# Kernel optimization log

Measured on AMD Instinct MI355X. Metric: run time of the kernel, lower is better.

The kernel has to match this reference:

```python
import jax, jax.numpy as jnp
import numpy as np

N, E, H, R = 20000, 320000, 64, 32
CUTOFF = 5.0
EYE3 = jnp.eye(3, dtype=jnp.float32)


def _decompose(X):
    # X: [..., 3, 3] -> (I trace part, A antisymmetric, S traceless symmetric)
    tr = jnp.trace(X, axis1=-2, axis2=-1)
    I = tr[..., None, None] / 3.0 * EYE3
    A = (X - jnp.swapaxes(X, -1, -2)) / 2.0
    S = (X + jnp.swapaxes(X, -1, -2)) / 2.0 - I
    return I, A, S


def _tnorm(X):
    return (X ** 2).sum((-2, -1))


def _mix(T, W):
    # channel-wise Linear without bias: Linear applied after permute(0,2,3,1)
    return jnp.einsum('nhij,gh->ngij', T, W)


def setup_inputs() -> dict:
    key = jax.random.key(0)
    ks = jax.random.split(key, 8)
    s = 0.05
    X = jax.random.normal(ks[0], (N, H, 3, 3), jnp.float32)
    edge_index = jax.random.randint(ks[1], (2, E), 0, N, dtype=jnp.int64)
    edge_dist = jax.random.uniform(ks[2], (E,), jnp.float32) * CUTOFF
    edge_attr = jax.random.normal(ks[3], (E, R), jnp.float32)
    w1 = jax.random.normal(ks[4], (H, R), jnp.float32) * s
    b1 = jnp.zeros((H,), jnp.float32)
    w2 = jax.random.normal(ks[5], (2 * H, H), jnp.float32) * s
    b2 = jnp.zeros((2 * H,), jnp.float32)
    w3 = jax.random.normal(ks[6], (3 * H, 2 * H), jnp.float32) * s
    b3 = jnp.zeros((3 * H,), jnp.float32)
    lin_w = jax.random.normal(ks[7], (6, H, H), jnp.float32) * s
    return dict(X=X, edge_index=edge_index, edge_dist=edge_dist, edge_attr=edge_attr,
                w1=w1, b1=b1, w2=w2, b2=b2, w3=w3, b3=b3, lin_w=lin_w)


def reference(X, edge_index, edge_dist, edge_attr, w1, b1, w2, b2, w3, b3, lin_w):
    row, col = edge_index[0], edge_index[1]
    # CosineCutoff: 0.5*(cos(pi*d/cutoff)+1) inside cutoff
    C = 0.5 * (jnp.cos(edge_dist * (jnp.pi / CUTOFF)) + 1.0) * (edge_dist < CUTOFF).astype(edge_dist.dtype)
    h = jax.nn.silu(edge_attr @ w1.T + b1)
    h = jax.nn.silu(h @ w2.T + b2)
    edge_feat = ((h @ w3.T + b3) * C[:, None]).reshape(E, H, 3)
    Xn = X / (_tnorm(X) + 1.0)[..., None, None]
    I, A, S = _decompose(Xn)
    I = _mix(I, lin_w[0])
    A = _mix(A, lin_w[1])
    S = _mix(S, lin_w[2])
    Y = I + A + S

    def msg(f, T):  # gather tensor[col], weight by edge factor, scatter-add to row
        return jax.ops.segment_sum(f[:, :, None, None] * T[col], row, num_segments=N)

    M = msg(edge_feat[..., 0], I) + msg(edge_feat[..., 1], A) + msg(edge_feat[..., 2], S)
    prod = jnp.matmul(M, Y) + jnp.matmul(Y, M)  # O(3) branch
    I2, A2, S2 = _decompose(prod)
    norm = (_tnorm(I2 + A2 + S2) + 1.0)[..., None, None]
    dX = _mix(I2 / norm, lin_w[3]) + _mix(A2 / norm, lin_w[4]) + _mix(S2 / norm, lin_w[5])
    return Xn + dX + jnp.matmul(dX, dX)
```

## Files before the change

### kernel.cpp

```cpp
#include <hip/hip_runtime.h>
#include <hip/hip_fp16.h>
#include <hip/hip_bf16.h>

#define NR 32

typedef __attribute__((ext_vector_type(8))) short bf8_t;
typedef __attribute__((ext_vector_type(4))) float f4_t;

__device__ __forceinline__ float silu_f(float x) {
    return x * __builtin_amdgcn_rcpf(1.0f + __expf(-x));
}

__device__ __forceinline__ unsigned pkbf(float lo, float hi) {
    __hip_bfloat162 h = __float22bfloat162_rn(make_float2(lo, hi));
    union { __hip_bfloat162 h2; unsigned u; } cv; cv.h2 = h; return cv.u;
}
__device__ __forceinline__ float bf_lo(unsigned u) { return __uint_as_float(u << 16); }
__device__ __forceinline__ float bf_hi(unsigned u) { return __uint_as_float(u & 0xffff0000u); }

__device__ __forceinline__ float rdl(float v, int l) {
    return __int_as_float(__builtin_amdgcn_readlane(__float_as_int(v), l));
}

__global__ __launch_bounds__(256) void k_hist(
    const int* __restrict__ eidx, int* __restrict__ cnt, int nedges)
{
    int e = blockIdx.x * 256 + threadIdx.x;
    if (e < nedges) atomicAdd(&cnt[eidx[e]], 1);
}

__global__ __launch_bounds__(256) void k_scatter(
    const int* __restrict__ eidx, int* __restrict__ cur,
    int* __restrict__ perm, int* __restrict__ col_s, int nedges)
{
    int e = blockIdx.x * 256 + threadIdx.x;
    if (e < nedges) {
        int r = eidx[e];
        int pos = atomicAdd(&cur[r], 1);
        perm[pos] = e;
        col_s[pos] = eidx[nedges + e];
    }
}

__global__ __launch_bounds__(512) void k_mega(
    int* __restrict__ cnt, int* __restrict__ off, int nnodes,
    const float* __restrict__ w1, const float* __restrict__ b1,
    const float* __restrict__ w2, const float* __restrict__ b2,
    const float* __restrict__ w3, const float* __restrict__ b3,
    unsigned* __restrict__ wpre,
    const float* __restrict__ X, const float* __restrict__ lw,
    unsigned* __restrict__ Tmh, int nk1blocks)
{
    __shared__ float Wl[3 * 64 * 68];
    const int tid = threadIdx.x;
    const int bid = blockIdx.x;

    if (bid == 0) {
        int* ish = (int*)Wl;
        const int lane = tid & 63, wid = tid >> 6;
        const int n = nnodes;
        const int per = (n + 511) >> 9;
        const int base = tid * per;
        int s = 0;
        for (int i = 0; i < per; i++) {
            int idx = base + i;
            if (idx < n) s += cnt[idx];
        }
        int incl = s;
        for (int d = 1; d < 64; d <<= 1) {
            int t = __shfl_up(incl, d);
            if (lane >= d) incl += t;
        }
        if (lane == 63) ish[wid] = incl;
        __syncthreads();
        if (wid == 0) {
            int v = (lane < 8) ? ish[lane] : 0;
            int inc2 = v;
            for (int d = 1; d < 8; d <<= 1) {
                int t = __shfl_up(inc2, d);
                if (lane >= d) inc2 += t;
            }
            if (lane < 8) ish[8 + lane] = inc2 - v;
            if (lane == 7) off[n] = inc2;
        }
        __syncthreads();
        int run = ish[8 + wid] + incl - s;
        for (int i = 0; i < per; i++) {
            int idx = base + i;
            if (idx < n) {
                int v = cnt[idx];
                off[idx] = run;
                cnt[idx] = run;
                run += v;
            }
        }
        return;
    }

    if (bid > nk1blocks) {
        int i = (bid - nk1blocks - 1) * 512 + tid;
        if (i < 12288) {
            int mk = i >> 8, m = mk >> 2, kt = mk & 3;
            int rr = (i >> 4) & 15, gg = (i >> 2) & 3, dd = i & 3;
            int row = 16 * m + rr;
            int c0 = 32 * kt + 16 * (dd >> 1) + 4 * gg + 2 * (dd & 1);
            const float* s = w3 + (size_t)row * 128 + c0;
            wpre[i] = pkbf(s[0], s[1]);
        } else if (i < 12672) {
            int j = i - 12288;
            float v = (j < 64) ? b1[j] : (j < 192) ? b2[j - 64] : b3[j - 192];
            wpre[i] = __float_as_uint(v);
        } else if (i < 13696) {
            int j = i - 12672;
            int m = j >> 8, rr = (j >> 4) & 15, gg = (j >> 2) & 3, dd = j & 3;
            const float* s = w1 + (size_t)(16 * m + rr) * 32 + 8 * gg + 2 * dd;
            wpre[i] = pkbf(s[0], s[1]);
        } else if (i < 17792) {
            int j = i - 13696;
            int mk = j >> 8, m = mk >> 1, kt = mk & 1;
            int rr = (j >> 4) & 15, gg = (j >> 2) & 3, dd = j & 3;
            int row = 16 * m + rr;
            int c0 = 32 * kt + 16 * (dd >> 1) + 4 * gg + 2 * (dd & 1);
            const float* s = w2 + (size_t)row * 64 + c0;
            wpre[i] = pkbf(s[0], s[1]);
        }
        return;
    }

#pragma unroll
    for (int k = 0; k < 6; k++) {
        int l = (tid + k * 512) * 4;
        int row = l >> 6, col = l & 63;
        *(float4*)&Wl[row * 68 + col] = *(const float4*)(lw + l);
    }

    const int wid = tid >> 6, lane = tid & 63;
    const int n = (bid - 1) * 8 + wid;
    const bool valid = (n < nnodes);

    float i0 = 0, i1 = 0, i2 = 0, i3 = 0, i4 = 0, i5 = 0, i6 = 0, i7 = 0, i8 = 0;
    if (valid) {
        const float* xp = X + ((size_t)n * 64 + lane) * 9;
        float v[9];
#pragma unroll
        for (int i = 0; i < 9; i++) v[i] = xp[i];
        float tn = 0.f;
#pragma unroll
        for (int i = 0; i < 9; i++) tn = fmaf(v[i], v[i], tn);
        float inv = 1.0f / (tn + 1.0f);
#pragma unroll
        for (int i = 0; i < 9; i++) v[i] *= inv;
        float lam = (v[0] + v[4] + v[8]) * (1.0f / 3.0f);
        i0 = lam;
        i1 = (v[1] - v[3]) * 0.5f;
        i2 = (v[2] - v[6]) * 0.5f;
        i3 = (v[5] - v[7]) * 0.5f;
        i4 = v[0] - lam;
        i5 = (v[1] + v[3]) * 0.5f;
        i6 = (v[2] + v[6]) * 0.5f;
        i7 = v[4] - lam;
        i8 = (v[5] + v[7]) * 0.5f;
    }
    __syncthreads();

    const int g = lane;
    float a0 = 0, a1 = 0, a2 = 0, a3 = 0, a4 = 0, a5 = 0, a6 = 0, a7 = 0, a8 = 0;
#pragma unroll
    for (int h4 = 0; h4 < 64; h4 += 4) {
        float4 w0 = *(const float4*)&Wl[g * 68 + h4];
        float4 w1v = *(const float4*)&Wl[(64 + g) * 68 + h4];
        float4 w2v = *(const float4*)&Wl[(128 + g) * 68 + h4];
#pragma unroll
        for (int j = 0; j < 4; j++) {
            const int h = h4 + j;
            float wa = (&w0.x)[j], wb = (&w1v.x)[j], wc = (&w2v.x)[j];
            a0 = fmaf(wa, rdl(i0, h), a0);
            a1 = fmaf(wb, rdl(i1, h), a1);
            a2 = fmaf(wb, rdl(i2, h), a2);
            a3 = fmaf(wb, rdl(i3, h), a3);
            a4 = fmaf(wc, rdl(i4, h), a4);
            a5 = fmaf(wc, rdl(i5, h), a5);
            a6 = fmaf(wc, rdl(i6, h), a6);
            a7 = fmaf(wc, rdl(i7, h), a7);
            a8 = fmaf(wc, rdl(i8, h), a8);
        }
    }
    if (valid) {
        unsigned* outp = Tmh + (size_t)n * 320 + g;
        outp[0 * 64] = pkbf(a0, a1);
        outp[1 * 64] = pkbf(a2, a3);
        outp[2 * 64] = pkbf(a4, a5);
        outp[3 * 64] = pkbf(a6, a7);
        outp[4 * 64] = pkbf(a8, 0.f);
    }
}

#define LBI 49152
#define LW1P 50688
#define LW2P 54784
#define LEF 71168
#define EFS 408
#define NW  14

__global__
__attribute__((amdgpu_flat_work_group_size(896, 896)))
__attribute__((amdgpu_waves_per_eu(3)))
void k2f_fused(
    const float* __restrict__ ea, const float* __restrict__ dist,
    const int* __restrict__ perm, const int* __restrict__ col_s,
    const int* __restrict__ off, const unsigned* __restrict__ wpre,
    const unsigned* __restrict__ Tmh, float* __restrict__ out, int nrows)
{
    __shared__ __align__(16) char smem[LEF + NW * 16 * EFS];
    const int tid = threadIdx.x;

#pragma unroll
    for (int k = 0; k < 5; k++) {
        int idx = tid + k * 896;
        if (idx < 4448)
            ((uint4*)smem)[idx] = ((const uint4*)wpre)[idx];
    }

    const int wid = tid >> 6, lane = tid & 63;
    const int r16 = lane & 15, g = lane >> 4;
    const int slot = r16 * 4 + g;
    char* efb = smem + LEF + wid * (16 * EFS);
    __syncthreads();

    const int r = blockIdx.x * NW + wid;
    if (r >= nrows) return;
    const int beg = off[r];
    const int deg = off[r + 1] - beg;

    float acc[9];
#pragma unroll
    for (int i = 0; i < 9; i++) acc[i] = 0.f;

#pragma unroll 1
    for (int c0 = 0; c0 < deg; c0 += 16) {
        const int cnt = min(16, deg - c0);

        int colv = col_s[beg + c0 + ((r16 < cnt) ? r16 : (cnt - 1))];
        int e = perm[beg + c0 + ((r16 < cnt) ? r16 : 0)];
        const float* ar = ea + (size_t)e * NR + 8 * g;
        float4 v0 = *(const float4*)(ar);
        float4 v1 = *(const float4*)(ar + 4);
        float d = dist[e];

        bf8_t bx;
        {
            union { bf8_t v; unsigned u[4]; } tt;
            tt.u[0] = pkbf(v0.x, v0.y); tt.u[1] = pkbf(v0.z, v0.w);
            tt.u[2] = pkbf(v1.x, v1.y); tt.u[3] = pkbf(v1.z, v1.w);
            bx = tt.v;
        }
        float cf = (r16 < cnt && d < 5.0f)
                 ? 0.5f * (__cosf(d * 0.62831853071795864f) + 1.0f) : 0.0f;

        unsigned pk1[4][2];
#pragma unroll
        for (int m = 0; m < 4; m++) {
            f4_t c = *(const f4_t*)(smem + LBI + (16 * m + 4 * g) * 4);
            bf8_t aw = *(const bf8_t*)(smem + LW1P + (m * 64 + slot) * 16);
            c = __builtin_amdgcn_mfma_f32_16x16x32_bf16(aw, bx, c, 0, 0, 0);
            pk1[m][0] = pkbf(silu_f(c[0]), silu_f(c[1]));
            pk1[m][1] = pkbf(silu_f(c[2]), silu_f(c[3]));
        }
        bf8_t B2[2];
        {
            union { bf8_t v; unsigned u[4]; } ta, tb;
            ta.u[0] = pk1[0][0]; ta.u[1] = pk1[0][1]; ta.u[2] = pk1[1][0]; ta.u[3] = pk1[1][1];
            tb.u[0] = pk1[2][0]; tb.u[1] = pk1[2][1]; tb.u[2] = pk1[3][0]; tb.u[3] = pk1[3][1];
            B2[0] = ta.v; B2[1] = tb.v;
        }

        unsigned pk2[8][2];
#pragma unroll
        for (int m = 0; m < 8; m++) {
            f4_t c = *(const f4_t*)(smem + LBI + (64 + 16 * m + 4 * g) * 4);
#pragma unroll
            for (int kt = 0; kt < 2; kt++) {
                bf8_t aw = *(const bf8_t*)(smem + LW2P + ((m * 2 + kt) * 64 + slot) * 16);
                c = __builtin_amdgcn_mfma_f32_16x16x32_bf16(aw, B2[kt], c, 0, 0, 0);
            }
            pk2[m][0] = pkbf(silu_f(c[0]), silu_f(c[1]));
            pk2[m][1] = pkbf(silu_f(c[2]), silu_f(c[3]));
        }
        bf8_t B3[4];
#pragma unroll
        for (int kt = 0; kt < 4; kt++) {
            union { bf8_t v; unsigned u[4]; } tt;
            tt.u[0] = pk2[2 * kt][0]; tt.u[1] = pk2[2 * kt][1];
            tt.u[2] = pk2[2 * kt + 1][0]; tt.u[3] = pk2[2 * kt + 1][1];
            B3[kt] = tt.v;
        }

        asm volatile("s_waitcnt lgkmcnt(0)" ::: "memory");
        __builtin_amdgcn_sched_barrier(0);

#pragma unroll
        for (int m = 0; m < 12; m++) {
            f4_t c = *(const f4_t*)(smem + LBI + (192 + 16 * m + 4 * g) * 4);
#pragma unroll
            for (int kt = 0; kt < 4; kt++) {
                bf8_t aw = *(const bf8_t*)(smem + ((m * 4 + kt) * 64 + slot) * 16);
                c = __builtin_amdgcn_mfma_f32_16x16x32_bf16(aw, B3[kt], c, 0, 0, 0);
            }
            union { struct { __half2 a, b; } h; uint2 u; } pu;
            pu.h.a = __float22half2_rn(make_float2(c[0] * cf, c[1] * cf));
            pu.h.b = __float22half2_rn(make_float2(c[2] * cf, c[3] * cf));
            *(uint2*)(efb + r16 * EFS + (16 * m + 4 * g) * 2) = pu.u;
        }
        asm volatile("s_waitcnt lgkmcnt(0)" ::: "memory");
        __builtin_amdgcn_sched_barrier(0);

        unsigned q[4][5];
#pragma unroll
        for (int s = 0; s < 4; s++) {
            int sc = __builtin_amdgcn_readlane(colv, s);
            const unsigned* t = Tmh + (size_t)(unsigned)sc * 320 + lane;
            q[s][0] = t[0]; q[s][1] = t[64]; q[s][2] = t[128];
            q[s][3] = t[192]; q[s][4] = t[256];
        }

#define ACC_STEP(S, Q)                                                        \
        {                                                                     \
            const __half* fp = (const __half*)(efb + (S) * EFS + 6 * lane);   \
            float f0 = __half2float(fp[0]);                                   \
            float f1 = __half2float(fp[1]);                                   \
            float f2 = __half2float(fp[2]);                                   \
            acc[0] = fmaf(f0, bf_lo(Q[0]), acc[0]);                           \
            acc[1] = fmaf(f1, bf_hi(Q[0]), acc[1]);                           \
            acc[2] = fmaf(f1, bf_lo(Q[1]), acc[2]);                           \
            acc[3] = fmaf(f1, bf_hi(Q[1]), acc[3]);                           \
            acc[4] = fmaf(f2, bf_lo(Q[2]), acc[4]);                           \
            acc[5] = fmaf(f2, bf_hi(Q[2]), acc[5]);                           \
            acc[6] = fmaf(f2, bf_lo(Q[3]), acc[6]);                           \
            acc[7] = fmaf(f2, bf_hi(Q[3]), acc[7]);                           \
            acc[8] = fmaf(f2, bf_lo(Q[4]), acc[8]);                           \
        }
#define LOAD_Q(DST, S)                                                        \
        {                                                                     \
            int sc = __builtin_amdgcn_readlane(colv, (S));                    \
            const unsigned* t = Tmh + (size_t)(unsigned)sc * 320 + lane;      \
            DST[0] = t[0]; DST[1] = t[64]; DST[2] = t[128];                   \
            DST[3] = t[192]; DST[4] = t[256];                                 \
        }

        ACC_STEP(0, q[0])  LOAD_Q(q[0], 4)
        ACC_STEP(1, q[1])  LOAD_Q(q[1], 5)
        ACC_STEP(2, q[2])  LOAD_Q(q[2], 6)
        ACC_STEP(3, q[3])  LOAD_Q(q[3], 7)
        ACC_STEP(4, q[0])  LOAD_Q(q[0], 8)
        ACC_STEP(5, q[1])  LOAD_Q(q[1], 9)
        ACC_STEP(6, q[2])  LOAD_Q(q[2], 10)
        ACC_STEP(7, q[3])  LOAD_Q(q[3], 11)
        ACC_STEP(8, q[0])  LOAD_Q(q[0], 12)
        ACC_STEP(9, q[1])  LOAD_Q(q[1], 13)
        ACC_STEP(10, q[2]) LOAD_Q(q[2], 14)
        ACC_STEP(11, q[3]) LOAD_Q(q[3], 15)
        ACC_STEP(12, q[0]) ACC_STEP(13, q[1]) ACC_STEP(14, q[2]) ACC_STEP(15, q[3])
#undef ACC_STEP
#undef LOAD_Q
    }

    float y[9];
    {
        const unsigned* tp = Tmh + (size_t)r * 320 + lane;
        unsigned q0 = tp[0], q1 = tp[64], q2 = tp[128], q3 = tp[192], q4 = tp[256];
        y[0] = bf_lo(q0); y[1] = bf_hi(q0); y[2] = bf_lo(q1); y[3] = bf_hi(q1);
        y[4] = bf_lo(q2); y[5] = bf_hi(q2); y[6] = bf_lo(q3); y[7] = bf_hi(q3);
        y[8] = bf_lo(q4);
    }
    float Y[9], Mm[9];
    Y[0] = y[0] + y[4]; Y[1] = y[1] + y[5]; Y[2] = y[2] + y[6];
    Y[3] = -y[1] + y[5]; Y[4] = y[0] + y[7]; Y[5] = y[3] + y[8];
    Y[6] = -y[2] + y[6]; Y[7] = -y[3] + y[8]; Y[8] = y[0] - y[4] - y[7];
    Mm[0] = acc[0] + acc[4]; Mm[1] = acc[1] + acc[5]; Mm[2] = acc[2] + acc[6];
    Mm[3] = -acc[1] + acc[5]; Mm[4] = acc[0] + acc[7]; Mm[5] = acc[3] + acc[8];
    Mm[6] = -acc[2] + acc[6]; Mm[7] = -acc[3] + acc[8]; Mm[8] = acc[0] - acc[4] - acc[7];
    float P[9];
#pragma unroll
    for (int a = 0; a < 3; a++)
#pragma unroll
        for (int b = 0; b < 3; b++) {
            float s = 0.f;
#pragma unroll
            for (int c = 0; c < 3; c++) {
                s = fmaf(Mm[a * 3 + c], Y[c * 3 + b], s);
                s = fmaf(Y[a * 3 + c], Mm[c * 3 + b], s);
            }
            P[a * 3 + b] = s;
        }
    float tn = 0.f;
#pragma unroll
    for (int k = 0; k < 9; k++) tn = fmaf(P[k], P[k], tn);
    float inv = 1.0f / (tn + 1.0f);
    float lam = (P[0] + P[4] + P[8]) * (1.0f / 3.0f);

    float* mp = out + (size_t)r * 576 + lane;
    mp[0 * 64] = lam * inv;
    mp[1 * 64] = (P[1] - P[3]) * 0.5f * inv;
    mp[2 * 64] = (P[2] - P[6]) * 0.5f * inv;
    mp[3 * 64] = (P[5] - P[7]) * 0.5f * inv;
    mp[4 * 64] = (P[0] - lam) * inv;
    mp[5 * 64] = (P[1] + P[3]) * 0.5f * inv;
    mp[6 * 64] = (P[2] + P[6]) * 0.5f * inv;
    mp[7 * 64] = (P[4] - lam) * inv;
    mp[8 * 64] = (P[5] + P[7]) * 0.5f * inv;
}

__global__ __launch_bounds__(512) void k4_final(
    const float* __restrict__ X, const float* __restrict__ lw,
    float* __restrict__ out, int nnodes)
{
    __shared__ float Wl[3 * 64 * 68];
    const int tid = threadIdx.x;
#pragma unroll
    for (int k = 0; k < 6; k++) {
        int l = (tid + k * 512) * 4;
        int row = l >> 6, col = l & 63;
        *(float4*)&Wl[row * 68 + col] = *(const float4*)(lw + 3 * 4096 + l);
    }

    const int wid = tid >> 6, lane = tid & 63;
    const int n = blockIdx.x * 8 + wid;
    const bool valid = (n < nnodes);

    float i0 = 0, i1 = 0, i2 = 0, i3 = 0, i4 = 0, i5 = 0, i6 = 0, i7 = 0, i8 = 0;
    if (valid) {
        const float* pp = out + (size_t)n * 576 + lane;
        i0 = pp[0 * 64]; i1 = pp[1 * 64]; i2 = pp[2 * 64];
        i3 = pp[3 * 64]; i4 = pp[4 * 64]; i5 = pp[5 * 64];
        i6 = pp[6 * 64]; i7 = pp[7 * 64]; i8 = pp[8 * 64];
    }
    __syncthreads();

    const int g = lane;
    float a0 = 0, a1 = 0, a2 = 0, a3 = 0, a4 = 0, a5 = 0, a6 = 0, a7 = 0, a8 = 0;
#pragma unroll
    for (int h4 = 0; h4 < 64; h4 += 4) {
        float4 w0 = *(const float4*)&Wl[g * 68 + h4];
        float4 w1 = *(const float4*)&Wl[(64 + g) * 68 + h4];
        float4 w2 = *(const float4*)&Wl[(128 + g) * 68 + h4];
#pragma unroll
        for (int j = 0; j < 4; j++) {
            const int h = h4 + j;
            float wa = (&w0.x)[j], wb = (&w1.x)[j], wc = (&w2.x)[j];
            a0 = fmaf(wa, rdl(i0, h), a0);
            a1 = fmaf(wb, rdl(i1, h), a1);
            a2 = fmaf(wb, rdl(i2, h), a2);
            a3 = fmaf(wb, rdl(i3, h), a3);
            a4 = fmaf(wc, rdl(i4, h), a4);
            a5 = fmaf(wc, rdl(i5, h), a5);
            a6 = fmaf(wc, rdl(i6, h), a6);
            a7 = fmaf(wc, rdl(i7, h), a7);
            a8 = fmaf(wc, rdl(i8, h), a8);
        }
    }

    if (valid) {
        float D[9];
        D[0] = a0 + a4; D[1] = a1 + a5; D[2] = a2 + a6;
        D[3] = -a1 + a5; D[4] = a0 + a7; D[5] = a3 + a8;
        D[6] = -a2 + a6; D[7] = -a3 + a8; D[8] = a0 - a4 - a7;

        const float* xp = X + ((size_t)n * 64 + g) * 9;
        float xv[9];
#pragma unroll
        for (int i = 0; i < 9; i++) xv[i] = xp[i];
        float tn = 0.f;
#pragma unroll
        for (int i = 0; i < 9; i++) tn = fmaf(xv[i], xv[i], tn);
        float inv = 1.0f / (tn + 1.0f);

        float* op = out + ((size_t)n * 64 + g) * 9;
        float res[9];
#pragma unroll
        for (int a = 0; a < 3; a++)
#pragma unroll
            for (int b = 0; b < 3; b++) {
                float dd = 0.f;
#pragma unroll
                for (int c = 0; c < 3; c++) dd = fmaf(D[a * 3 + c], D[c * 3 + b], dd);
                res[a * 3 + b] = xv[a * 3 + b] * inv + D[a * 3 + b] + dd;
            }
#pragma unroll
        for (int i = 0; i < 9; i++) op[i] = res[i];
    }
}

extern "C" void kernel_launch(void* const* d_in, const int* in_sizes, int n_in,
                              void* d_out, int out_size, void* d_ws, size_t ws_size,
                              hipStream_t stream)
{
    const float* X    = (const float*)d_in[0];
    const int*   eidx = (const int*)d_in[1];
    const float* dist = (const float*)d_in[2];
    const float* ea   = (const float*)d_in[3];
    const float* w1   = (const float*)d_in[4];
    const float* b1   = (const float*)d_in[5];
    const float* w2   = (const float*)d_in[6];
    const float* b2   = (const float*)d_in[7];
    const float* w3   = (const float*)d_in[8];
    const float* b3   = (const float*)d_in[9];
    const float* lw   = (const float*)d_in[10];
    float* outp = (float*)d_out;

    const int nnodes = in_sizes[0] / (64 * 9);
    const int nedges = in_sizes[2];

    unsigned* Tmh  = (unsigned*)d_ws;
    int* cur       = (int*)(Tmh + (size_t)nnodes * 320);
    int* off       = cur + nnodes;
    int* perm      = off + nnodes + 1;
    int* col_s     = perm + nedges;
    unsigned* wpre = (unsigned*)(col_s + nedges);

    const int nk1 = (nnodes + 7) / 8;
    const int nprep = (17792 + 511) / 512;

    hipMemsetAsync(cur, 0, (size_t)nnodes * sizeof(int), stream);
    k_hist<<<(nedges + 255) / 256, 256, 0, stream>>>(eidx, cur, nedges);
    k_mega<<<1 + nk1 + nprep, 512, 0, stream>>>(cur, off, nnodes,
                                                w1, b1, w2, b2, w3, b3, wpre,
                                                X, lw, Tmh, nk1);
    k_scatter<<<(nedges + 255) / 256, 256, 0, stream>>>(eidx, cur, perm, col_s, nedges);

    k2f_fused<<<(nnodes + NW - 1) / NW, 64 * NW, 0, stream>>>(ea, dist, perm, col_s, off, wpre, Tmh, outp, nnodes);
    k4_final<<<(nnodes + 7) / 8, 512, 0, stream>>>(X, lw, outp, nnodes);
}
```

Before: 353.3 us.

## Fuse final channel-mix and output kernel into edge aggregation kernel

The final k4_final kernel is folded into k2f_fused. Each wave now keeps its normalized I/A/S components in registers, reloads the lw[3..5] weights into the reused shared memory, and computes the channel mix plus Xn + dX + dX·dX directly. This removes one kernel launch and the 576-float-per-node intermediate write and readback through global memory. In exchange it adds two block-wide barriers, lets out-of-range waves stay alive, adds a per-block weight reload into LDS, and may raise register pressure in an already heavy kernel.

```diff
diff --git a/kernel.cpp b/kernel.cpp
--- a/kernel.cpp
+++ b/kernel.cpp
@@ -209,7 +209,9 @@
     const float* __restrict__ ea, const float* __restrict__ dist,
     const int* __restrict__ perm, const int* __restrict__ col_s,
     const int* __restrict__ off, const unsigned* __restrict__ wpre,
-    const unsigned* __restrict__ Tmh, float* __restrict__ out, int nrows)
+    const unsigned* __restrict__ Tmh,
+    const float* __restrict__ X, const float* __restrict__ lw3,
+    float* __restrict__ out, int nrows)
 {
     __shared__ __align__(16) char smem[LEF + NW * 16 * EFS];
     const int tid = threadIdx.x;
@@ -228,9 +230,9 @@
     __syncthreads();
 
     const int r = blockIdx.x * NW + wid;
-    if (r >= nrows) return;
-    const int beg = off[r];
-    const int deg = off[r + 1] - beg;
+    const int rc = (r < nrows) ? r : 0;
+    int beg = 0, deg = 0;
+    if (r < nrows) { beg = off[r]; deg = off[r + 1] - beg; }
 
     float acc[9];
 #pragma unroll
@@ -366,7 +368,7 @@
 
     float y[9];
     {
-        const unsigned* tp = Tmh + (size_t)r * 320 + lane;
+        const unsigned* tp = Tmh + (size_t)rc * 320 + lane;
         unsigned q0 = tp[0], q1 = tp[64], q2 = tp[128], q3 = tp[192], q4 = tp[256];
         y[0] = bf_lo(q0); y[1] = bf_hi(q0); y[2] = bf_lo(q1); y[3] = bf_hi(q1);
         y[4] = bf_lo(q2); y[5] = bf_hi(q2); y[6] = bf_lo(q3); y[7] = bf_hi(q3);
@@ -398,55 +400,35 @@
     float inv = 1.0f / (tn + 1.0f);
     float lam = (P[0] + P[4] + P[8]) * (1.0f / 3.0f);
 
-    float* mp = out + (size_t)r * 576 + lane;
-    mp[0 * 64] = lam * inv;
-    mp[1 * 64] = (P[1] - P[3]) * 0.5f * inv;
-    mp[2 * 64] = (P[2] - P[6]) * 0.5f * inv;
-    mp[3 * 64] = (P[5] - P[7]) * 0.5f * inv;
-    mp[4 * 64] = (P[0] - lam) * inv;
-    mp[5 * 64] = (P[1] + P[3]) * 0.5f * inv;
-    mp[6 * 64] = (P[2] + P[6]) * 0.5f * inv;
-    mp[7 * 64] = (P[4] - lam) * inv;
-    mp[8 * 64] = (P[5] + P[7]) * 0.5f * inv;
-}
-
-__global__ __launch_bounds__(512) void k4_final(
-    const float* __restrict__ X, const float* __restrict__ lw,
-    float* __restrict__ out, int nnodes)
-{
-    __shared__ float Wl[3 * 64 * 68];
-    const int tid = threadIdx.x;
-#pragma unroll
-    for (int k = 0; k < 6; k++) {
-        int l = (tid + k * 512) * 4;
-        int row = l >> 6, col = l & 63;
-        *(float4*)&Wl[row * 68 + col] = *(const float4*)(lw + 3 * 4096 + l);
-    }
-
-    const int wid = tid >> 6, lane = tid & 63;
-    const int n = blockIdx.x * 8 + wid;
-    const bool valid = (n < nnodes);
-
-    float i0 = 0, i1 = 0, i2 = 0, i3 = 0, i4 = 0, i5 = 0, i6 = 0, i7 = 0, i8 = 0;
-    if (valid) {
-        const float* pp = out + (size_t)n * 576 + lane;
-        i0 = pp[0 * 64]; i1 = pp[1 * 64]; i2 = pp[2 * 64];
-        i3 = pp[3 * 64]; i4 = pp[4 * 64]; i5 = pp[5 * 64];
-        i6 = pp[6 * 64]; i7 = pp[7 * 64]; i8 = pp[8 * 64];
-    }
+    float i0 = lam * inv;
+    float i1 = (P[1] - P[3]) * 0.5f * inv;
+    float i2 = (P[2] - P[6]) * 0.5f * inv;
+    float i3 = (P[5] - P[7]) * 0.5f * inv;
+    float i4 = (P[0] - lam) * inv;
+    float i5 = (P[1] + P[3]) * 0.5f * inv;
+    float i6 = (P[2] + P[6]) * 0.5f * inv;
+    float i7 = (P[4] - lam) * inv;
+    float i8 = (P[5] + P[7]) * 0.5f * inv;
+
     __syncthreads();
-
-    const int g = lane;
+    float* Wl = (float*)smem;
+    for (int idx = tid; idx < 12288; idx += 896) {
+        int row = idx >> 6, col = idx & 63;
+        Wl[row * 68 + col] = lw3[idx];
+    }
+    __syncthreads();
+
+    const int gch = lane;
     float a0 = 0, a1 = 0, a2 = 0, a3 = 0, a4 = 0, a5 = 0, a6 = 0, a7 = 0, a8 = 0;
 #pragma unroll
     for (int h4 = 0; h4 < 64; h4 += 4) {
-        float4 w0 = *(const float4*)&Wl[g * 68 + h4];
-        float4 w1 = *(const float4*)&Wl[(64 + g) * 68 + h4];
-        float4 w2 = *(const float4*)&Wl[(128 + g) * 68 + h4];
+        float4 w0 = *(const float4*)&Wl[gch * 68 + h4];
+        float4 w1v = *(const float4*)&Wl[(64 + gch) * 68 + h4];
+        float4 w2v = *(const float4*)&Wl[(128 + gch) * 68 + h4];
 #pragma unroll
         for (int j = 0; j < 4; j++) {
             const int h = h4 + j;
-            float wa = (&w0.x)[j], wb = (&w1.x)[j], wc = (&w2.x)[j];
+            float wa = (&w0.x)[j], wb = (&w1v.x)[j], wc = (&w2v.x)[j];
             a0 = fmaf(wa, rdl(i0, h), a0);
             a1 = fmaf(wb, rdl(i1, h), a1);
             a2 = fmaf(wb, rdl(i2, h), a2);
@@ -459,22 +441,22 @@
         }
     }
 
-    if (valid) {
+    if (r < nrows) {
         float D[9];
         D[0] = a0 + a4; D[1] = a1 + a5; D[2] = a2 + a6;
         D[3] = -a1 + a5; D[4] = a0 + a7; D[5] = a3 + a8;
         D[6] = -a2 + a6; D[7] = -a3 + a8; D[8] = a0 - a4 - a7;
 
-        const float* xp = X + ((size_t)n * 64 + g) * 9;
+        const float* xp = X + ((size_t)r * 64 + gch) * 9;
         float xv[9];
 #pragma unroll
         for (int i = 0; i < 9; i++) xv[i] = xp[i];
-        float tn = 0.f;
-#pragma unroll
-        for (int i = 0; i < 9; i++) tn = fmaf(xv[i], xv[i], tn);
-        float inv = 1.0f / (tn + 1.0f);
-
-        float* op = out + ((size_t)n * 64 + g) * 9;
+        float tn2 = 0.f;
+#pragma unroll
+        for (int i = 0; i < 9; i++) tn2 = fmaf(xv[i], xv[i], tn2);
+        float inv2 = 1.0f / (tn2 + 1.0f);
+
+        float* op = out + ((size_t)r * 64 + gch) * 9;
         float res[9];
 #pragma unroll
         for (int a = 0; a < 3; a++)
@@ -483,7 +465,7 @@
                 float dd = 0.f;
 #pragma unroll
                 for (int c = 0; c < 3; c++) dd = fmaf(D[a * 3 + c], D[c * 3 + b], dd);
-                res[a * 3 + b] = xv[a * 3 + b] * inv + D[a * 3 + b] + dd;
+                res[a * 3 + b] = xv[a * 3 + b] * inv2 + D[a * 3 + b] + dd;
             }
 #pragma unroll
         for (int i = 0; i < 9; i++) op[i] = res[i];
@@ -527,6 +509,6 @@
                                                 X, lw, Tmh, nk1);
     k_scatter<<<(nedges + 255) / 256, 256, 0, stream>>>(eidx, cur, perm, col_s, nedges);
 
-    k2f_fused<<<(nnodes + NW - 1) / NW, 64 * NW, 0, stream>>>(ea, dist, perm, col_s, off, wpre, Tmh, outp, nnodes);
-    k4_final<<<(nnodes + 7) / 8, 512, 0, stream>>>(X, lw, outp, nnodes);
-}
+    k2f_fused<<<(nnodes + NW - 1) / NW, 64 * NW, 0, stream>>>(ea, dist, perm, col_s, off, wpre,
+                                                              Tmh, X, lw + 3 * 4096, outp, nnodes);
+}
```

After: 392.3 us. +11.1%, slower.
